# Kernel optimization log

Hardware: AMD Instinct MI355X
Metric: run time of the kernel (lower is better)

The kernel has to match this reference:

```python
import jax, jax.numpy as jnp
import numpy as np

NS = 150  # MC weight samples


def setup_inputs() -> dict:
    key = jax.random.key(0)
    mu_shapes = {
        'mu_W0': (512, 784), 'mu_b0': (512,),
        'mu_W1': (512, 512), 'mu_b1': (512,),
        'mu_W2': (512, 512), 'mu_b2': (512,),
        'mu_W3': (10, 512),  'mu_b3': (10,),
    }
    ks = list(jax.random.split(key, 2 * len(mu_shapes) + 1))
    inp = {'x': jax.random.normal(ks[0], (64, 784), jnp.float32)}
    i = 1
    for name, shp in mu_shapes.items():
        inp[name] = jax.random.normal(ks[i], shp, jnp.float32) * 0.05
        i += 1
    for name, shp in mu_shapes.items():
        # log-std around -3 => std ~ 0.05
        inp['v_' + name[3:]] = jax.random.normal(ks[i], shp, jnp.float32) * 0.1 - 3.0
        i += 1
    return inp


def _sample(k, mu, v):
    # original: r = randn_like(m) * sqrt(exp(2*v)) == randn * exp(v); param = r + m
    eps = jax.random.normal(k, (NS,) + mu.shape, mu.dtype)
    return mu + jnp.exp(v) * eps  # [NS, *mu.shape]


def reference(x, mu_W0, mu_b0, mu_W1, mu_b1, mu_W2, mu_b2, mu_W3, mu_b3,
              v_W0, v_b0, v_W1, v_b1, v_W2, v_b2, v_W3, v_b3):
    ks = jax.random.split(jax.random.key(1), 8)
    W0 = _sample(ks[0], mu_W0, v_W0); b0 = _sample(ks[1], mu_b0, v_b0)
    W1 = _sample(ks[2], mu_W1, v_W1); b1 = _sample(ks[3], mu_b1, v_b1)
    W2 = _sample(ks[4], mu_W2, v_W2); b2 = _sample(ks[5], mu_b2, v_b2)
    W3 = _sample(ks[6], mu_W3, v_W3); b3 = _sample(ks[7], mu_b3, v_b3)
    # batched-over-samples MLP forward: s = sample, b = batch
    h = jax.nn.relu(jnp.einsum('bi,soi->sbo', x, W0) + b0[:, None, :])
    h = jax.nn.relu(jnp.einsum('sbi,soi->sbo', h, W1) + b1[:, None, :])
    h = jax.nn.relu(jnp.einsum('sbi,soi->sbo', h, W2) + b2[:, None, :])
    out = jnp.einsum('sbi,soi->sbo', h, W3) + b3[:, None, :]  # [NS, B, 10]
    return out
```

## Files before the change

### kernel.cpp

```cpp
#include <hip/hip_runtime.h>


typedef short bf16x8 __attribute__((ext_vector_type(8)));
typedef int   i32x4  __attribute__((ext_vector_type(4)));
typedef float f32x4  __attribute__((ext_vector_type(4)));

#define TF_R(r) { x0 += x1; x1 = (x1 << (r)) | (x1 >> (32 - (r))); x1 ^= x0; }

#define TF8(r) { _Pragma("unroll") for (int j = 0; j < 8; ++j) { \
    a[j] += b[j]; b[j] = (b[j] << (r)) | (b[j] >> (32 - (r))); b[j] ^= a[j]; } }
#define INJ8(kka, kkb) { _Pragma("unroll") for (int j = 0; j < 8; ++j) { \
    a[j] += (kka); b[j] += (kkb); } }

__device__ __forceinline__ unsigned int tf_xor(unsigned int k0, unsigned int k1,
                                               unsigned int c1)
{
  const unsigned int ks2 = k0 ^ k1 ^ 0x1BD11BDAu;
  unsigned int x0 = k0;
  unsigned int x1 = c1 + k1;
  TF_R(13) TF_R(15) TF_R(26) TF_R(6)
  x0 += k1;  x1 += ks2 + 1u;
  TF_R(17) TF_R(29) TF_R(16) TF_R(24)
  x0 += ks2; x1 += k0 + 2u;
  TF_R(13) TF_R(15) TF_R(26) TF_R(6)
  x0 += k0;  x1 += k1 + 3u;
  TF_R(17) TF_R(29) TF_R(16) TF_R(24)
  x0 += k1;  x1 += ks2 + 4u;
  TF_R(13) TF_R(15) TF_R(26) TF_R(6)
  x0 += ks2; x1 += k0 + 5u;
  return x0 ^ x1;
}

__device__ __forceinline__ float bits_to_g(unsigned int r)
{
  float f = __uint_as_float((r >> 9) | 0x3F800000u) - 1.0f;
  float x = __builtin_fmaf(f, 2.0f, -0.99999994f);
  float L = __log2f(__builtin_fmaf(-x, x, 1.0f));
  float t  = __builtin_fmaf(L, -0.6931472f, -2.5f);
  float p = -4.39150654e-06f;
  p = __builtin_fmaf(p, t, 0.00021858087f);
  p = __builtin_fmaf(p, t, -0.00125372503f);
  p = __builtin_fmaf(p, t, -0.00417768164f);
  p = __builtin_fmaf(p, t, 0.246640727f);
  p = __builtin_fmaf(p, t, 1.50140941f);
  if (__builtin_expect(L <= -7.2134752f, 0)) {
    float w  = L * -0.6931472f;
    float t2 = sqrtf(w) - 3.0f;
    float pt = 0.00573950773f;
    pt = __builtin_fmaf(pt, t2, -0.0076224613f);
    pt = __builtin_fmaf(pt, t2, 0.00943887047f);
    pt = __builtin_fmaf(pt, t2, 1.00167406f);
    pt = __builtin_fmaf(pt, t2, 2.83297682f);
    p = pt;
  }
  return p * x;
}

__device__ __forceinline__ unsigned short f32_to_bf16_rne(float v)
{
  unsigned int u = __float_as_uint(v);
  unsigned int r = (u + 0x7FFFu + ((u >> 16) & 1u)) >> 16;
  return (unsigned short)r;
}

__device__ __forceinline__ unsigned int pack_bf16_rne(float a, float b)
{
#if __has_builtin(__builtin_amdgcn_cvt_pk_bf16_f32)
  typedef __bf16 bf16x2_t __attribute__((ext_vector_type(2)));
  bf16x2_t r = __builtin_amdgcn_cvt_pk_bf16_f32(a, b);
  return __builtin_bit_cast(unsigned int, r);
#else
  unsigned int ua = __float_as_uint(a);
  unsigned int ub = __float_as_uint(b);
  ua += 0x7FFFu + ((ua >> 16) & 1u);
  ub += 0x7FFFu + ((ub >> 16) & 1u);
  return __builtin_amdgcn_perm(ub, ua, 0x07060302u);
#endif
}

__global__ __launch_bounds__(256) void xpad_kernel(const float* __restrict__ x,
                                                   unsigned short* __restrict__ xp)
{
  int i = blockIdx.x * 256 + threadIdx.x;
  if (i >= 64 * 832) return;
  int m = i / 832, k = i - m * 832;
  float v = (k < 784) ? x[m * 784 + k] : 0.0f;
  xp[i] = f32_to_bf16_rne(v);
}

__global__ __launch_bounds__(256) void pack_kernel(
    const float* __restrict__ muW0, const float* __restrict__ vW0,
    const float* __restrict__ muW1, const float* __restrict__ vW1,
    const float* __restrict__ muW2, const float* __restrict__ vW2,
    const float* __restrict__ muW3, const float* __restrict__ vW3,
    float2* __restrict__ msP0, float2* __restrict__ msP1,
    float2* __restrict__ msP2, float2* __restrict__ msP3)
{
  int b = blockIdx.x, tid = threadIdx.x;
  const float* mu; const float* v; float2* o;
  int KV, NV, osh, base;
  if (b < 1664)      { mu = muW0; v = vW0; o = msP0; KV = 784; NV = 512; osh = 9; base = 0;    }
  else if (b < 2688) { mu = muW1; v = vW1; o = msP1; KV = 512; NV = 512; osh = 9; base = 1664; }
  else if (b < 3712) { mu = muW2; v = vW2; o = msP2; KV = 512; NV = 512; osh = 9; base = 2688; }
  else               { mu = muW3; v = vW3; o = msP3; KV = 512; NV = 10;  osh = 4; base = 3712; }
  int e = (b - base) * 256 + tid;
  int k = (e & 7) | ((e >> (3 + osh)) << 3);
  int n = (e >> 3) & ((1 << osh) - 1);
  float2 r = {0.0f, 0.0f};
  if (k < KV && n < NV) {
    r.x = mu[n * KV + k];
    r.y = __expf(v[n * KV + k]) * 1.41421356237f;
  }
  o[e] = r;
}

__global__ __launch_bounds__(256) void bias_kernel(
    const float* __restrict__ mu0, const float* __restrict__ v0, float* __restrict__ o0,
    const float* __restrict__ mu1, const float* __restrict__ v1, float* __restrict__ o1,
    const float* __restrict__ mu2, const float* __restrict__ v2, float* __restrict__ o2,
    const float* __restrict__ mu3, const float* __restrict__ v3, float* __restrict__ o3,
    unsigned int k00, unsigned int k01, unsigned int k10, unsigned int k11,
    unsigned int k20, unsigned int k21, unsigned int k30, unsigned int k31)
{
  int b = blockIdx.x, tid = threadIdx.x;
  int seg = b / 300; if (seg > 3) seg = 3;
  const float* mu; const float* v; float* o; unsigned int ka, kb; int n;
  if      (seg == 0) { mu = mu0; v = v0; o = o0; ka = k00; kb = k01; n = 76800; }
  else if (seg == 1) { mu = mu1; v = v1; o = o1; ka = k10; kb = k11; n = 76800; }
  else if (seg == 2) { mu = mu2; v = v2; o = o2; ka = k20; kb = k21; n = 76800; }
  else               { mu = mu3; v = v3; o = o3; ka = k30; kb = k31; n = 1500;  }
  int e = (b - seg * 300) * 256 + tid;
  if (e >= n) return;
  int oo = (seg == 3) ? (e % 10) : (e & 511);
  float eps = 1.41421356237f * bits_to_g(tf_xor(ka, kb, (unsigned int)e));
  o[e] = __builtin_fmaf(__expf(v[oo]), eps, mu[oo]);
}

__global__ __launch_bounds__(256) void bias3_out(float* __restrict__ Out,
                                                 const float* __restrict__ b3s)
{
  int i = blockIdx.x * 256 + threadIdx.x;
  if (i >= 96000) return;
  int s = i / 640;
  int rem = i - s * 640;
  int n = rem % 10;
  Out[i] = b3s[s * 10 + n];
}

template<int KVALID, int KPAD, int ASTRIDE, int AROW>
__global__
__attribute__((amdgpu_flat_work_group_size(256, 256)))
__attribute__((amdgpu_waves_per_eu(1, 4)))
void layer_fused(
    const unsigned short* __restrict__ A,
    unsigned short* __restrict__ Out,
    const float2* __restrict__ msP,
    const float* __restrict__ bS,
    unsigned int k0, unsigned int k1)
{
  constexpr int NSTEPS = KPAD / 32;
  constexpr int OVALID = 512, OPITCH = 512;
  const unsigned int ks2 = k0 ^ k1 ^ 0x1BD11BDAu;
  const int s    = blockIdx.y;
  const int tid  = threadIdx.x;
  const int wave = tid >> 6, lane = tid & 63;
  const int quad = lane >> 4;
  const int n16  = lane & 15;
  const int nlane = blockIdx.x * 16 + n16;

  const unsigned short* As = A + (size_t)s * ASTRIDE;
  const unsigned int idx_base = (unsigned int)s * (unsigned int)(OVALID * KVALID)
                              + (unsigned int)nlane * (unsigned int)KVALID;

  f32x4 acc[4] = {f32x4{0,0,0,0}, f32x4{0,0,0,0}, f32x4{0,0,0,0}, f32x4{0,0,0,0}};

  auto load_step = [&](int st, bf16x8 (&af)[4], float4 (&q)[4]) {
    const int kb = st * 32 + quad * 8;
    #pragma unroll
    for (int mt = 0; mt < 4; ++mt)
      af[mt] = *reinterpret_cast<const bf16x8*>(
          As + (size_t)(mt * 16 + n16) * AROW + kb);
    const float4* mp = reinterpret_cast<const float4*>(
        msP + ((size_t)(kb >> 3) * OPITCH + nlane) * 8);
    #pragma unroll
    for (int h = 0; h < 4; ++h)
      q[h] = mp[h];
  };

  auto compute_step = [&](int st, bf16x8 (&af)[4], float4 (&q)[4]) {
    const int kb = st * 32 + quad * 8;
    unsigned int a[8], b[8];
    const unsigned int cb = idx_base + (unsigned int)kb + k1;
    #pragma unroll
    for (int j = 0; j < 8; ++j) { a[j] = k0; b[j] = cb + (unsigned int)j; }
    TF8(13) TF8(15) TF8(26) TF8(6)  INJ8(k1, ks2 + 1u)
    TF8(17) TF8(29) TF8(16) TF8(24) INJ8(ks2, k0 + 2u)
    TF8(13) TF8(15) TF8(26) TF8(6)  INJ8(k0, k1 + 3u)
    TF8(17) TF8(29) TF8(16) TF8(24) INJ8(k1, ks2 + 4u)
    TF8(13) TF8(15) TF8(26) TF8(6)  INJ8(ks2, k0 + 5u)

    float g[8];
    #pragma unroll
    for (int j = 0; j < 8; ++j)
      g[j] = bits_to_g(a[j] ^ b[j]);

    float wv[8];
    wv[0] = __builtin_fmaf(q[0].y, g[0], q[0].x);
    wv[1] = __builtin_fmaf(q[0].w, g[1], q[0].z);
    wv[2] = __builtin_fmaf(q[1].y, g[2], q[1].x);
    wv[3] = __builtin_fmaf(q[1].w, g[3], q[1].z);
    wv[4] = __builtin_fmaf(q[2].y, g[4], q[2].x);
    wv[5] = __builtin_fmaf(q[2].w, g[5], q[2].z);
    wv[6] = __builtin_fmaf(q[3].y, g[6], q[3].x);
    wv[7] = __builtin_fmaf(q[3].w, g[7], q[3].z);

    i32x4 bp;
    #pragma unroll
    for (int h = 0; h < 4; ++h)
      bp[h] = (int)pack_bf16_rne(wv[2 * h], wv[2 * h + 1]);
    bf16x8 bfrag = __builtin_bit_cast(bf16x8, bp);

    #pragma unroll
    for (int mt = 0; mt < 4; ++mt)
      acc[mt] = __builtin_amdgcn_mfma_f32_16x16x32_bf16(af[mt], bfrag, acc[mt], 0, 0, 0);
  };

  bf16x8 afA[4], afB[4];
  float4 qA[4], qB[4];
  int st = wave;
  if (st < NSTEPS) load_step(st, afA, qA);
  while (st < NSTEPS) {
    int n1 = st + 4;
    if (n1 < NSTEPS) load_step(n1, afB, qB);
    __builtin_amdgcn_sched_barrier(0);
    compute_step(st, afA, qA);
    st = n1;
    if (st >= NSTEPS) break;
    int n2 = st + 4;
    if (n2 < NSTEPS) load_step(n2, afA, qA);
    __builtin_amdgcn_sched_barrier(0);
    compute_step(st, afB, qB);
    st = n2;
  }

  __shared__ float red[4 * 16 * 64];
  #pragma unroll
  for (int mt = 0; mt < 4; ++mt)
    #pragma unroll
    for (int r = 0; r < 4; ++r)
      red[(wave * 16 + mt * 4 + r) * 64 + lane] = acc[mt][r];
  __syncthreads();

  const int m   = tid >> 2;
  const int nq  = (tid & 3) * 4;
  const int row = (m >> 4) * 4 + (m & 3);
  const int col = ((m >> 2) & 3) * 16 + nq;

  float4 p0 = *reinterpret_cast<const float4*>(&red[(0 * 16 + row) * 64 + col]);
  float4 p1 = *reinterpret_cast<const float4*>(&red[(1 * 16 + row) * 64 + col]);
  float4 p2 = *reinterpret_cast<const float4*>(&red[(2 * 16 + row) * 64 + col]);
  float4 p3 = *reinterpret_cast<const float4*>(&red[(3 * 16 + row) * 64 + col]);
  float v0 = (p0.x + p1.x) + (p2.x + p3.x);
  float v1 = (p0.y + p1.y) + (p2.y + p3.y);
  float v2 = (p0.z + p1.z) + (p2.z + p3.z);
  float v3 = (p0.w + p1.w) + (p2.w + p3.w);

  const float4 b4 = *reinterpret_cast<const float4*>(
      &bS[s * OVALID + blockIdx.x * 16 + nq]);
  float o0 = fmaxf(v0 + b4.x, 0.0f), o1 = fmaxf(v1 + b4.y, 0.0f);
  float o2 = fmaxf(v2 + b4.z, 0.0f), o3 = fmaxf(v3 + b4.w, 0.0f);
  uint2 stv;
  stv.x = pack_bf16_rne(o0, o1);
  stv.y = pack_bf16_rne(o2, o3);
  *reinterpret_cast<uint2*>(
      Out + ((size_t)s * 64 + m) * OPITCH + blockIdx.x * 16 + nq) = stv;
}

__global__ __launch_bounds__(256) void layer3_atomic(
    const unsigned short* __restrict__ A,
    float* __restrict__ Out,
    const float2* __restrict__ msP,
    unsigned int k0, unsigned int k1)
{
  const unsigned int ks2 = k0 ^ k1 ^ 0x1BD11BDAu;
  const int s    = blockIdx.y;
  const int tid  = threadIdx.x;
  const int wave = tid >> 6, lane = tid & 63;
  const int quad = lane >> 4;
  const int n    = lane & 15;

  const unsigned short* As = A + (size_t)s * (64 * 512);
  const int st = blockIdx.x * 4 + wave;
  const int kb = st * 32 + quad * 8;
  const unsigned int idx_base = (unsigned int)s * 5120u + (unsigned int)n * 512u;

  const float4* mp = reinterpret_cast<const float4*>(
      msP + ((size_t)(kb >> 3) * 16 + n) * 8);
  float4 q0 = mp[0], q1 = mp[1], q2 = mp[2], q3 = mp[3];

  unsigned int a[8], b[8];
  const unsigned int cb = idx_base + (unsigned int)kb + k1;
  #pragma unroll
  for (int j = 0; j < 8; ++j) { a[j] = k0; b[j] = cb + (unsigned int)j; }
  TF8(13) TF8(15) TF8(26) TF8(6)  INJ8(k1, ks2 + 1u)
  TF8(17) TF8(29) TF8(16) TF8(24) INJ8(ks2, k0 + 2u)
  TF8(13) TF8(15) TF8(26) TF8(6)  INJ8(k0, k1 + 3u)
  TF8(17) TF8(29) TF8(16) TF8(24) INJ8(k1, ks2 + 4u)
  TF8(13) TF8(15) TF8(26) TF8(6)  INJ8(ks2, k0 + 5u)

  float g[8];
  #pragma unroll
  for (int j = 0; j < 8; ++j)
    g[j] = bits_to_g(a[j] ^ b[j]);

  float wv[8];
  wv[0] = __builtin_fmaf(q0.y, g[0], q0.x);
  wv[1] = __builtin_fmaf(q0.w, g[1], q0.z);
  wv[2] = __builtin_fmaf(q1.y, g[2], q1.x);
  wv[3] = __builtin_fmaf(q1.w, g[3], q1.z);
  wv[4] = __builtin_fmaf(q2.y, g[4], q2.x);
  wv[5] = __builtin_fmaf(q2.w, g[5], q2.z);
  wv[6] = __builtin_fmaf(q3.y, g[6], q3.x);
  wv[7] = __builtin_fmaf(q3.w, g[7], q3.z);

  i32x4 bp;
  #pragma unroll
  for (int h = 0; h < 4; ++h)
    bp[h] = (int)pack_bf16_rne(wv[2 * h], wv[2 * h + 1]);
  bf16x8 bfrag = __builtin_bit_cast(bf16x8, bp);

  f32x4 acc[4] = {f32x4{0,0,0,0}, f32x4{0,0,0,0}, f32x4{0,0,0,0}, f32x4{0,0,0,0}};
  #pragma unroll
  for (int mt = 0; mt < 4; ++mt) {
    bf16x8 afrag = *reinterpret_cast<const bf16x8*>(
        As + (size_t)(mt * 16 + n) * 512 + kb);
    acc[mt] = __builtin_amdgcn_mfma_f32_16x16x32_bf16(afrag, bfrag, acc[mt], 0, 0, 0);
  }

  __shared__ float red[4 * 16 * 64];
  #pragma unroll
  for (int mt = 0; mt < 4; ++mt)
    #pragma unroll
    for (int r = 0; r < 4; ++r)
      red[(wave * 16 + mt * 4 + r) * 64 + lane] = acc[mt][r];
  __syncthreads();

  const int m   = tid >> 2;
  const int nq  = (tid & 3) * 4;
  const int row = (m >> 4) * 4 + (m & 3);
  const int col = ((m >> 2) & 3) * 16 + nq;

  float4 p0 = *reinterpret_cast<const float4*>(&red[(0 * 16 + row) * 64 + col]);
  float4 p1 = *reinterpret_cast<const float4*>(&red[(1 * 16 + row) * 64 + col]);
  float4 p2 = *reinterpret_cast<const float4*>(&red[(2 * 16 + row) * 64 + col]);
  float4 p3 = *reinterpret_cast<const float4*>(&red[(3 * 16 + row) * 64 + col]);
  float vv[4];
  vv[0] = (p0.x + p1.x) + (p2.x + p3.x);
  vv[1] = (p0.y + p1.y) + (p2.y + p3.y);
  vv[2] = (p0.z + p1.z) + (p2.z + p3.z);
  vv[3] = (p0.w + p1.w) + (p2.w + p3.w);

  #pragma unroll
  for (int jj = 0; jj < 4; ++jj) {
    int nn = nq + jj;
    if (nn < 10)
      atomicAdd(&Out[((size_t)s * 64 + m) * 10 + nn], vv[jj]);
  }
}

static void tf_host(unsigned int k0, unsigned int k1, unsigned int c0, unsigned int c1,
                    unsigned int* o0, unsigned int* o1)
{
  const unsigned int ks2 = k0 ^ k1 ^ 0x1BD11BDAu;
  unsigned int x0 = c0 + k0, x1 = c1 + k1;
  TF_R(13) TF_R(15) TF_R(26) TF_R(6)
  x0 += k1;  x1 += ks2 + 1u;
  TF_R(17) TF_R(29) TF_R(16) TF_R(24)
  x0 += ks2; x1 += k0 + 2u;
  TF_R(13) TF_R(15) TF_R(26) TF_R(6)
  x0 += k0;  x1 += k1 + 3u;
  TF_R(17) TF_R(29) TF_R(16) TF_R(24)
  x0 += k1;  x1 += ks2 + 4u;
  TF_R(13) TF_R(15) TF_R(26) TF_R(6)
  x0 += ks2; x1 += k0 + 5u;
  *o0 = x0; *o1 = x1;
}

extern "C" void kernel_launch(void* const* d_in, const int* in_sizes, int n_in,
                              void* d_out, int out_size, void* d_ws, size_t ws_size,
                              hipStream_t stream)
{
  (void)in_sizes; (void)n_in; (void)out_size; (void)ws_size;

  const float* x    = (const float*)d_in[0];
  const float* muW0 = (const float*)d_in[1];
  const float* mub0 = (const float*)d_in[2];
  const float* muW1 = (const float*)d_in[3];
  const float* mub1 = (const float*)d_in[4];
  const float* muW2 = (const float*)d_in[5];
  const float* mub2 = (const float*)d_in[6];
  const float* muW3 = (const float*)d_in[7];
  const float* mub3 = (const float*)d_in[8];
  const float* vW0  = (const float*)d_in[9];
  const float* vb0  = (const float*)d_in[10];
  const float* vW1  = (const float*)d_in[11];
  const float* vb1  = (const float*)d_in[12];
  const float* vW2  = (const float*)d_in[13];
  const float* vb2  = (const float*)d_in[14];
  const float* vW3  = (const float*)d_in[15];
  const float* vb3  = (const float*)d_in[16];

  unsigned int key[8][2];
  for (unsigned int i = 0; i < 8; ++i)
    tf_host(0u, 1u, 0u, i, &key[i][0], &key[i][1]);

  char* ws = (char*)d_ws;
  unsigned short* xp = (unsigned short*)(ws);
  unsigned short* hA = (unsigned short*)(ws + 106496);
  float* b0s  = (float*)(ws + 9936896);
  float* b1s  = (float*)(ws + 10244096);
  float* b2s  = (float*)(ws + 10551296);
  float* b3s  = (float*)(ws + 10858496);
  float2* msP1 = (float2*)(ws + 10866688);
  float2* msP2 = (float2*)(ws + 12963840);
  float2* msP3 = (float2*)(ws + 15060992);
  float2* msP0 = (float2*)(ws + 15126528);
  unsigned short* hB = (unsigned short*)(ws + 15126528);

  xpad_kernel<<<208, 256, 0, stream>>>(x, xp);
  pack_kernel<<<3744, 256, 0, stream>>>(muW0, vW0, muW1, vW1, muW2, vW2, muW3, vW3,
                                        msP0, msP1, msP2, msP3);
  bias_kernel<<<906, 256, 0, stream>>>(mub0, vb0, b0s, mub1, vb1, b1s,
                                       mub2, vb2, b2s, mub3, vb3, b3s,
                                       key[1][0], key[1][1], key[3][0], key[3][1],
                                       key[5][0], key[5][1], key[7][0], key[7][1]);
  bias3_out<<<375, 256, 0, stream>>>((float*)d_out, b3s);

  layer_fused<784, 832, 0,     832><<<dim3(32, 150), 256, 0, stream>>>(
      xp, hA, msP0, b0s, key[0][0], key[0][1]);
  layer_fused<512, 512, 32768, 512><<<dim3(32, 150), 256, 0, stream>>>(
      hA, hB, msP1, b1s, key[2][0], key[2][1]);
  layer_fused<512, 512, 32768, 512><<<dim3(32, 150), 256, 0, stream>>>(
      hB, hA, msP2, b2s, key[4][0], key[4][1]);
  layer3_atomic<<<dim3(4, 150), 256, 0, stream>>>(
      hA, (float*)d_out, msP3, key[6][0], key[6][1]);
}
```

Measured before the change: 422.4 us.

## Pack FMA math, fold Threefry init rounds, trim layer-0 K padding

Rewrites the in-kernel Threefry generation so the first round and the key injections are folded algebraically, which saves integer ops per random value. The Gaussian transform and the weight FMA now use packed f32 instructions (v_pk_fma/v_pk_mul), with the mean/sigma layout shuffled into pairs to suit them, and bf16 conversion goes through inline asm. Layer 0's K padding shrinks from 832 to 800, which reduces both the padded work and the pack-kernel size. The main cost targeted is ALU-bound RNG and erfinv work inside the fused GEMM, at the risk of changing the padded-K tiling assumptions and relying on inline asm.

```diff
diff --git a/kernel.cpp b/kernel.cpp
--- a/kernel.cpp
+++ b/kernel.cpp
@@ -4,13 +4,55 @@
 typedef short bf16x8 __attribute__((ext_vector_type(8)));
 typedef int   i32x4  __attribute__((ext_vector_type(4)));
 typedef float f32x4  __attribute__((ext_vector_type(4)));
+typedef float f32x2  __attribute__((ext_vector_type(2)));
+
+__device__ __forceinline__ f32x2 mk2(float a, float b)
+{
+  f32x2 r; r.x = a; r.y = b; return r;
+}
+
+__device__ __forceinline__ f32x2 pk_fma(f32x2 a, f32x2 b, f32x2 c)
+{
+  f32x2 d;
+  asm("v_pk_fma_f32 %0, %1, %2, %3" : "=v"(d) : "v"(a), "v"(b), "v"(c));
+  return d;
+}
+__device__ __forceinline__ f32x2 pk_mul(f32x2 a, f32x2 b)
+{
+  f32x2 d;
+  asm("v_pk_mul_f32 %0, %1, %2" : "=v"(d) : "v"(a), "v"(b));
+  return d;
+}
+
+__device__ __forceinline__ unsigned int cvt_pk_bf16(float a, float b)
+{
+  unsigned int d;
+  asm("v_cvt_pk_bf16_f32 %0, %1, %2" : "=v"(d) : "v"(a), "v"(b));
+  return d;
+}
 
 #define TF_R(r) { x0 += x1; x1 = (x1 << (r)) | (x1 >> (32 - (r))); x1 ^= x0; }
 
 #define TF8(r) { _Pragma("unroll") for (int j = 0; j < 8; ++j) { \
     a[j] += b[j]; b[j] = (b[j] << (r)) | (b[j] >> (32 - (r))); b[j] ^= a[j]; } }
-#define INJ8(kka, kkb) { _Pragma("unroll") for (int j = 0; j < 8; ++j) { \
-    a[j] += (kka); b[j] += (kkb); } }
+#define ROTX8(r) { _Pragma("unroll") for (int j = 0; j < 8; ++j) { \
+    b[j] = ((b[j] << (r)) | (b[j] >> (32 - (r)))) ^ a[j]; } }
+#define INJM8(kka, kkb) { const unsigned int _ka = (kka), _kb = (kkb); \
+    _Pragma("unroll") for (int j = 0; j < 8; ++j) { \
+    b[j] += _kb; a[j] = a[j] + b[j] + _ka; } }
+
+#define TF8_FULL(rout) { \
+    const unsigned int _kc = cb + k0; \
+    _Pragma("unroll") for (int j = 0; j < 8; ++j) { \
+      b[j] = cb + (unsigned int)j; a[j] = _kc + (unsigned int)j; } \
+    ROTX8(13) TF8(15) TF8(26) TF8(6) \
+    INJM8(k1, ks2 + 1u)  ROTX8(17) TF8(29) TF8(16) TF8(24) \
+    INJM8(ks2, k0 + 2u)  ROTX8(13) TF8(15) TF8(26) TF8(6) \
+    INJM8(k0, k1 + 3u)   ROTX8(17) TF8(29) TF8(16) TF8(24) \
+    INJM8(k1, ks2 + 4u)  ROTX8(13) TF8(15) TF8(26) TF8(6) \
+    const unsigned int _f1 = k0 + 5u; \
+    _Pragma("unroll") for (int j = 0; j < 8; ++j) \
+      rout[j] = (a[j] + ks2) ^ (b[j] + _f1); }
 
 __device__ __forceinline__ unsigned int tf_xor(unsigned int k0, unsigned int k1,
                                                unsigned int c1)
@@ -31,9 +73,26 @@
   return x0 ^ x1;
 }
 
+__device__ __forceinline__ float erfinv_tail(float L)
+{
+  float w  = L * -0.6931472f;
+  float t2 = sqrtf(w) - 3.0f;
+  float pt = 0.00573950773f;
+  pt = __builtin_fmaf(pt, t2, -0.0076224613f);
+  pt = __builtin_fmaf(pt, t2, 0.00943887047f);
+  pt = __builtin_fmaf(pt, t2, 1.00167406f);
+  pt = __builtin_fmaf(pt, t2, 2.83297682f);
+  return pt;
+}
+
+__device__ __forceinline__ float bits_to_f(unsigned int r)
+{
+  return __uint_as_float(__builtin_amdgcn_alignbit(0x7Fu, r, 9u)) - 1.0f;
+}
+
 __device__ __forceinline__ float bits_to_g(unsigned int r)
 {
-  float f = __uint_as_float((r >> 9) | 0x3F800000u) - 1.0f;
+  float f = bits_to_f(r);
   float x = __builtin_fmaf(f, 2.0f, -0.99999994f);
   float L = __log2f(__builtin_fmaf(-x, x, 1.0f));
   float t  = __builtin_fmaf(L, -0.6931472f, -2.5f);
@@ -43,17 +102,30 @@
   p = __builtin_fmaf(p, t, -0.00417768164f);
   p = __builtin_fmaf(p, t, 0.246640727f);
   p = __builtin_fmaf(p, t, 1.50140941f);
-  if (__builtin_expect(L <= -7.2134752f, 0)) {
-    float w  = L * -0.6931472f;
-    float t2 = sqrtf(w) - 3.0f;
-    float pt = 0.00573950773f;
-    pt = __builtin_fmaf(pt, t2, -0.0076224613f);
-    pt = __builtin_fmaf(pt, t2, 0.00943887047f);
-    pt = __builtin_fmaf(pt, t2, 1.00167406f);
-    pt = __builtin_fmaf(pt, t2, 2.83297682f);
-    p = pt;
-  }
+  if (__builtin_expect(L <= -7.2134752f, 0))
+    p = erfinv_tail(L);
   return p * x;
+}
+
+__device__ __forceinline__ f32x2 bits_to_g2(unsigned int r0, unsigned int r1)
+{
+  float f0 = bits_to_f(r0);
+  float f1 = bits_to_f(r1);
+  f32x2 x = pk_fma(mk2(f0, f1), mk2(2.0f, 2.0f),
+                   mk2(-0.99999994f, -0.99999994f));
+  float L0 = __log2f(__builtin_fmaf(-x.x, x.x, 1.0f));
+  float L1 = __log2f(__builtin_fmaf(-x.y, x.y, 1.0f));
+  f32x2 t = pk_fma(mk2(L0, L1), mk2(-0.6931472f, -0.6931472f),
+                   mk2(-2.5f, -2.5f));
+  f32x2 p = mk2(-4.39150654e-06f, -4.39150654e-06f);
+  p = pk_fma(p, t, mk2(0.00021858087f, 0.00021858087f));
+  p = pk_fma(p, t, mk2(-0.00125372503f, -0.00125372503f));
+  p = pk_fma(p, t, mk2(-0.00417768164f, -0.00417768164f));
+  p = pk_fma(p, t, mk2(0.246640727f, 0.246640727f));
+  p = pk_fma(p, t, mk2(1.50140941f, 1.50140941f));
+  if (__builtin_expect(L0 <= -7.2134752f, 0)) p.x = erfinv_tail(L0);
+  if (__builtin_expect(L1 <= -7.2134752f, 0)) p.y = erfinv_tail(L1);
+  return pk_mul(p, x);
 }
 
 __device__ __forceinline__ unsigned short f32_to_bf16_rne(float v)
@@ -63,27 +135,12 @@
   return (unsigned short)r;
 }
 
-__device__ __forceinline__ unsigned int pack_bf16_rne(float a, float b)
-{
-#if __has_builtin(__builtin_amdgcn_cvt_pk_bf16_f32)
-  typedef __bf16 bf16x2_t __attribute__((ext_vector_type(2)));
-  bf16x2_t r = __builtin_amdgcn_cvt_pk_bf16_f32(a, b);
-  return __builtin_bit_cast(unsigned int, r);
-#else
-  unsigned int ua = __float_as_uint(a);
-  unsigned int ub = __float_as_uint(b);
-  ua += 0x7FFFu + ((ua >> 16) & 1u);
-  ub += 0x7FFFu + ((ub >> 16) & 1u);
-  return __builtin_amdgcn_perm(ub, ua, 0x07060302u);
-#endif
-}
-
 __global__ __launch_bounds__(256) void xpad_kernel(const float* __restrict__ x,
                                                    unsigned short* __restrict__ xp)
 {
   int i = blockIdx.x * 256 + threadIdx.x;
-  if (i >= 64 * 832) return;
-  int m = i / 832, k = i - m * 832;
+  if (i >= 64 * 800) return;
+  int m = i / 800, k = i - m * 800;
   float v = (k < 784) ? x[m * 784 + k] : 0.0f;
   xp[i] = f32_to_bf16_rne(v);
 }
@@ -99,18 +156,23 @@
   int b = blockIdx.x, tid = threadIdx.x;
   const float* mu; const float* v; float2* o;
   int KV, NV, osh, base;
-  if (b < 1664)      { mu = muW0; v = vW0; o = msP0; KV = 784; NV = 512; osh = 9; base = 0;    }
-  else if (b < 2688) { mu = muW1; v = vW1; o = msP1; KV = 512; NV = 512; osh = 9; base = 1664; }
-  else if (b < 3712) { mu = muW2; v = vW2; o = msP2; KV = 512; NV = 512; osh = 9; base = 2688; }
-  else               { mu = muW3; v = vW3; o = msP3; KV = 512; NV = 10;  osh = 4; base = 3712; }
+  if (b < 1600)      { mu = muW0; v = vW0; o = msP0; KV = 784; NV = 512; osh = 9; base = 0;    }
+  else if (b < 2624) { mu = muW1; v = vW1; o = msP1; KV = 512; NV = 512; osh = 9; base = 1600; }
+  else if (b < 3648) { mu = muW2; v = vW2; o = msP2; KV = 512; NV = 512; osh = 9; base = 2624; }
+  else               { mu = muW3; v = vW3; o = msP3; KV = 512; NV = 10;  osh = 4; base = 3648; }
   int e = (b - base) * 256 + tid;
   int k = (e & 7) | ((e >> (3 + osh)) << 3);
   int n = (e >> 3) & ((1 << osh) - 1);
-  float2 r = {0.0f, 0.0f};
+  float mu_v = 0.0f, sg_v = 0.0f;
   if (k < KV && n < NV) {
-    r.x = mu[n * KV + k];
-    r.y = __expf(v[n * KV + k]) * 1.41421356237f;
+    mu_v = mu[n * KV + k];
+    sg_v = __expf(v[n * KV + k]) * 1.41421356237f;
   }
+  float mu_o = __shfl_xor(mu_v, 1);
+  float sg_o = __shfl_xor(sg_v, 1);
+  float2 r;
+  if ((e & 1) == 0) { r.x = mu_v; r.y = mu_o; }
+  else              { r.x = sg_o; r.y = sg_v; }
   o[e] = r;
 }
 
@@ -189,35 +251,17 @@
 
   auto compute_step = [&](int st, bf16x8 (&af)[4], float4 (&q)[4]) {
     const int kb = st * 32 + quad * 8;
-    unsigned int a[8], b[8];
+    unsigned int a[8], b[8], r[8];
     const unsigned int cb = idx_base + (unsigned int)kb + k1;
-    #pragma unroll
-    for (int j = 0; j < 8; ++j) { a[j] = k0; b[j] = cb + (unsigned int)j; }
-    TF8(13) TF8(15) TF8(26) TF8(6)  INJ8(k1, ks2 + 1u)
-    TF8(17) TF8(29) TF8(16) TF8(24) INJ8(ks2, k0 + 2u)
-    TF8(13) TF8(15) TF8(26) TF8(6)  INJ8(k0, k1 + 3u)
-    TF8(17) TF8(29) TF8(16) TF8(24) INJ8(k1, ks2 + 4u)
-    TF8(13) TF8(15) TF8(26) TF8(6)  INJ8(ks2, k0 + 5u)
-
-    float g[8];
-    #pragma unroll
-    for (int j = 0; j < 8; ++j)
-      g[j] = bits_to_g(a[j] ^ b[j]);
-
-    float wv[8];
-    wv[0] = __builtin_fmaf(q[0].y, g[0], q[0].x);
-    wv[1] = __builtin_fmaf(q[0].w, g[1], q[0].z);
-    wv[2] = __builtin_fmaf(q[1].y, g[2], q[1].x);
-    wv[3] = __builtin_fmaf(q[1].w, g[3], q[1].z);
-    wv[4] = __builtin_fmaf(q[2].y, g[4], q[2].x);
-    wv[5] = __builtin_fmaf(q[2].w, g[5], q[2].z);
-    wv[6] = __builtin_fmaf(q[3].y, g[6], q[3].x);
-    wv[7] = __builtin_fmaf(q[3].w, g[7], q[3].z);
+    TF8_FULL(r)
 
     i32x4 bp;
     #pragma unroll
-    for (int h = 0; h < 4; ++h)
-      bp[h] = (int)pack_bf16_rne(wv[2 * h], wv[2 * h + 1]);
+    for (int h = 0; h < 4; ++h) {
+      f32x2 g2 = bits_to_g2(r[2 * h], r[2 * h + 1]);
+      f32x2 wv = pk_fma(mk2(q[h].z, q[h].w), g2, mk2(q[h].x, q[h].y));
+      bp[h] = (int)cvt_pk_bf16(wv.x, wv.y);
+    }
     bf16x8 bfrag = __builtin_bit_cast(bf16x8, bp);
 
     #pragma unroll
@@ -270,8 +314,8 @@
   float o0 = fmaxf(v0 + b4.x, 0.0f), o1 = fmaxf(v1 + b4.y, 0.0f);
   float o2 = fmaxf(v2 + b4.z, 0.0f), o3 = fmaxf(v3 + b4.w, 0.0f);
   uint2 stv;
-  stv.x = pack_bf16_rne(o0, o1);
-  stv.y = pack_bf16_rne(o2, o3);
+  stv.x = cvt_pk_bf16(o0, o1);
+  stv.y = cvt_pk_bf16(o2, o3);
   *reinterpret_cast<uint2*>(
       Out + ((size_t)s * 64 + m) * OPITCH + blockIdx.x * 16 + nq) = stv;
 }
@@ -296,37 +340,21 @@
 
   const float4* mp = reinterpret_cast<const float4*>(
       msP + ((size_t)(kb >> 3) * 16 + n) * 8);
-  float4 q0 = mp[0], q1 = mp[1], q2 = mp[2], q3 = mp[3];
-
-  unsigned int a[8], b[8];
+  float4 q[4];
+  #pragma unroll
+  for (int h = 0; h < 4; ++h) q[h] = mp[h];
+
+  unsigned int a[8], b[8], r[8];
   const unsigned int cb = idx_base + (unsigned int)kb + k1;
-  #pragma unroll
-  for (int j = 0; j < 8; ++j) { a[j] = k0; b[j] = cb + (unsigned int)j; }
-  TF8(13) TF8(15) TF8(26) TF8(6)  INJ8(k1, ks2 + 1u)
-  TF8(17) TF8(29) TF8(16) TF8(24) INJ8(ks2, k0 + 2u)
-  TF8(13) TF8(15) TF8(26) TF8(6)  INJ8(k0, k1 + 3u)
-  TF8(17) TF8(29) TF8(16) TF8(24) INJ8(k1, ks2 + 4u)
-  TF8(13) TF8(15) TF8(26) TF8(6)  INJ8(ks2, k0 + 5u)
-
-  float g[8];
-  #pragma unroll
-  for (int j = 0; j < 8; ++j)
-    g[j] = bits_to_g(a[j] ^ b[j]);
-
-  float wv[8];
-  wv[0] = __builtin_fmaf(q0.y, g[0], q0.x);
-  wv[1] = __builtin_fmaf(q0.w, g[1], q0.z);
-  wv[2] = __builtin_fmaf(q1.y, g[2], q1.x);
-  wv[3] = __builtin_fmaf(q1.w, g[3], q1.z);
-  wv[4] = __builtin_fmaf(q2.y, g[4], q2.x);
-  wv[5] = __builtin_fmaf(q2.w, g[5], q2.z);
-  wv[6] = __builtin_fmaf(q3.y, g[6], q3.x);
-  wv[7] = __builtin_fmaf(q3.w, g[7], q3.z);
+  TF8_FULL(r)
 
   i32x4 bp;
   #pragma unroll
-  for (int h = 0; h < 4; ++h)
-    bp[h] = (int)pack_bf16_rne(wv[2 * h], wv[2 * h + 1]);
+  for (int h = 0; h < 4; ++h) {
+    f32x2 g2 = bits_to_g2(r[2 * h], r[2 * h + 1]);
+    f32x2 wv = pk_fma(mk2(q[h].z, q[h].w), g2, mk2(q[h].x, q[h].y));
+    bp[h] = (int)cvt_pk_bf16(wv.x, wv.y);
+  }
   bf16x8 bfrag = __builtin_bit_cast(bf16x8, bp);
 
   f32x4 acc[4] = {f32x4{0,0,0,0}, f32x4{0,0,0,0}, f32x4{0,0,0,0}, f32x4{0,0,0,0}};
@@ -341,8 +369,8 @@
   #pragma unroll
   for (int mt = 0; mt < 4; ++mt)
     #pragma unroll
-    for (int r = 0; r < 4; ++r)
-      red[(wave * 16 + mt * 4 + r) * 64 + lane] = acc[mt][r];
+    for (int rr = 0; rr < 4; ++rr)
+      red[(wave * 16 + mt * 4 + rr) * 64 + lane] = acc[mt][rr];
   __syncthreads();
 
   const int m   = tid >> 2;
@@ -427,8 +455,8 @@
   float2* msP0 = (float2*)(ws + 15126528);
   unsigned short* hB = (unsigned short*)(ws + 15126528);
 
-  xpad_kernel<<<208, 256, 0, stream>>>(x, xp);
-  pack_kernel<<<3744, 256, 0, stream>>>(muW0, vW0, muW1, vW1, muW2, vW2, muW3, vW3,
+  xpad_kernel<<<200, 256, 0, stream>>>(x, xp);
+  pack_kernel<<<3680, 256, 0, stream>>>(muW0, vW0, muW1, vW1, muW2, vW2, muW3, vW3,
                                         msP0, msP1, msP2, msP3);
   bias_kernel<<<906, 256, 0, stream>>>(mub0, vb0, b0s, mub1, vb1, b1s,
                                        mub2, vb2, b2s, mub3, vb3, b3s,
@@ -436,7 +464,7 @@
                                        key[5][0], key[5][1], key[7][0], key[7][1]);
   bias3_out<<<375, 256, 0, stream>>>((float*)d_out, b3s);
 
-  layer_fused<784, 832, 0,     832><<<dim3(32, 150), 256, 0, stream>>>(
+  layer_fused<784, 800, 0,     800><<<dim3(32, 150), 256, 0, stream>>>(
       xp, hA, msP0, b0s, key[0][0], key[0][1]);
   layer_fused<512, 512, 32768, 512><<<dim3(32, 150), 256, 0, stream>>>(
       hA, hB, msP1, b1s, key[2][0], key[2][1]);
```

Measured after the change: 417.7 us. Within noise of the previous version (-1.1%).
